# Optimization experiments

Measured on AMD Instinct MI355X. Metric: run time of the kernel, lower is better.

Reference implementation:

```python
import jax, jax.numpy as jnp
import numpy as np

N_HEAD = 16
D_MODEL = 1024
T_DIM = 64
# Faithful to torch source: temperature = d_model // n_head ** 0.5  ==  d_model // (n_head**0.5)
TEMPERATURE = D_MODEL // (N_HEAD ** 0.5)  # 1024 // 4.0 = 256.0
LN_EPS = 1e-5


def setup_inputs() -> dict:
    key = jax.random.key(0)
    ks = jax.random.split(key, 10)
    B, S = 4, 2048
    w = 0.02  # weight scale to keep activations/logits in a sane range
    return {
        "q": jax.random.normal(ks[0], (B, S, D_MODEL), jnp.float32),
        "k": jax.random.normal(ks[1], (B, S, D_MODEL), jnp.float32),
        "v": jax.random.normal(ks[2], (B, S, D_MODEL), jnp.float32),
        "t": jax.random.normal(ks[3], (B, T_DIM), jnp.float32),
        "w_q": jax.random.normal(ks[4], (D_MODEL, D_MODEL), jnp.float32) * w,
        "w_k": jax.random.normal(ks[5], (D_MODEL, D_MODEL), jnp.float32) * w,
        "w_v": jax.random.normal(ks[6], (D_MODEL, D_MODEL), jnp.float32) * w,
        "w_fc": jax.random.normal(ks[7], (D_MODEL, D_MODEL), jnp.float32) * w,
        "ada_w": jax.random.normal(ks[8], (2 * D_MODEL, T_DIM), jnp.float32) * w,
        "ada_b": jax.random.normal(ks[9], (2 * D_MODEL,), jnp.float32) * w,
    }


def _ada_layer_norm(x, t_emb, ada_w, ada_b):
    # linear(gelu(t_emb)) -> [B, 2*d]; exact (erf) GELU as in torch nn.GELU default
    emb = jax.nn.gelu(t_emb, approximate=False) @ ada_w.T + ada_b
    emb = emb[:, None, :]  # [B, 1, 2*d]
    scale, shift = jnp.split(emb, 2, axis=-1)
    mean = jnp.mean(x, axis=-1, keepdims=True)
    var = jnp.var(x, axis=-1, keepdims=True)
    ln = (x - mean) * jax.lax.rsqrt(var + LN_EPS)
    return ln * (1.0 + scale) + shift


def reference(q, k, v, t, w_q, w_k, w_v, w_fc, ada_w, ada_b):
    B, Sq, D = q.shape
    Sk = k.shape[1]
    H, Dk = N_HEAD, D // N_HEAD

    q = _ada_layer_norm(q, t, ada_w, ada_b)
    residual = q

    # projections (torch Linear, no bias): y = x @ W.T
    qh = (q @ w_q.T).reshape(B, Sq, H, Dk).transpose(0, 2, 1, 3)  # [B,H,Sq,Dk]
    kh = (k @ w_k.T).reshape(B, Sk, H, Dk).transpose(0, 2, 1, 3)
    vh = (v @ w_v.T).reshape(B, Sk, H, Dk).transpose(0, 2, 1, 3)

    scores = jnp.einsum("bhqd,bhkd->bhqk", qh, kh) / TEMPERATURE
    attn = jax.nn.softmax(scores, axis=-1)
    out = jnp.einsum("bhqk,bhkd->bhqd", attn, vh)  # [B,H,Sq,Dk]

    out = out.transpose(0, 2, 1, 3).reshape(B, Sq, D)
    out = out @ w_fc.T  # dropout is identity in eval
    return out + residual
```

## Files before the change

kernel.cpp:

```cpp
#include <hip/hip_runtime.h>
#include <hip/hip_bf16.h>
#include <cstdint>

typedef short bf16x8 __attribute__((ext_vector_type(8)));
typedef float f32x4  __attribute__((ext_vector_type(4)));
typedef unsigned short u16x8 __attribute__((ext_vector_type(8)));
typedef unsigned short u16x4 __attribute__((ext_vector_type(4)));

#define SEQ    2048
#define BATCH  4
#define DMODEL 1024
#define NHEAD  16
#define DKH    64
#define MROWS  (BATCH * SEQ)

__device__ __forceinline__ unsigned short f2bf(float f) {
  union { float f; uint32_t u; } x; x.f = f;
  uint32_t r = (x.u + 0x7fffu + ((x.u >> 16) & 1u)) >> 16;
  return (unsigned short)r;
}
__device__ __forceinline__ float bf2f(unsigned short u) {
  union { uint32_t u; float f; } x; x.u = ((uint32_t)u) << 16;
  return x.f;
}
__device__ __forceinline__ void gload_lds16(const void* g, void* l) {
  __builtin_amdgcn_global_load_lds(
      (const __attribute__((address_space(1))) void*)g,
      (__attribute__((address_space(3))) void*)l, 16, 0, 0);
}

__global__ __launch_bounds__(256) void cast_f32_bf16(
    const float* __restrict__ in, unsigned short* __restrict__ out, int n) {
  int i = (blockIdx.x * 256 + threadIdx.x) * 4;
  if (i + 3 < n) {
    float4 v = *(const float4*)(in + i);
    u16x4 o;
    o[0] = f2bf(v.x); o[1] = f2bf(v.y); o[2] = f2bf(v.z); o[3] = f2bf(v.w);
    *(u16x4*)(out + i) = o;
  }
}

__global__ __launch_bounds__(256) void ada_emb_kernel(
    const float* __restrict__ t, const float* __restrict__ ada_w,
    const float* __restrict__ ada_b, float* __restrict__ emb) {
  int b = blockIdx.y;
  int j = blockIdx.x * 256 + threadIdx.x;
  __shared__ float g[64];
  if (threadIdx.x < 64) {
    float x = t[b * 64 + threadIdx.x];
    g[threadIdx.x] = x * 0.5f * (1.0f + erff(x * 0.70710678118654752f));
  }
  __syncthreads();
  float acc = ada_b[j];
  const float* wr = ada_w + (size_t)j * 64;
  #pragma unroll
  for (int i = 0; i < 64; ++i) acc += g[i] * wr[i];
  emb[b * 2048 + j] = acc;
}

__global__ __launch_bounds__(256) void adaln_kernel(
    const float* __restrict__ q, const float* __restrict__ emb,
    unsigned short* __restrict__ xbf) {
  int row = blockIdx.x;
  int b = row >> 11;
  int tid = threadIdx.x;
  float4 x = ((const float4*)(q + (size_t)row * DMODEL))[tid];
  float s  = x.x + x.y + x.z + x.w;
  float s2 = x.x * x.x + x.y * x.y + x.z * x.z + x.w * x.w;
  #pragma unroll
  for (int off = 32; off > 0; off >>= 1) {
    s  += __shfl_down(s, off);
    s2 += __shfl_down(s2, off);
  }
  __shared__ float red[8];
  int w = tid >> 6;
  if ((tid & 63) == 0) { red[w * 2] = s; red[w * 2 + 1] = s2; }
  __syncthreads();
  s  = red[0] + red[2] + red[4] + red[6];
  s2 = red[1] + red[3] + red[5] + red[7];
  float mean = s * (1.0f / 1024.0f);
  float var  = s2 * (1.0f / 1024.0f) - mean * mean;
  float rs = rsqrtf(var + 1e-5f);
  float4 sc = ((const float4*)(emb + (size_t)b * 2048))[tid];
  float4 sh = ((const float4*)(emb + (size_t)b * 2048 + 1024))[tid];
  u16x4 o;
  o[0] = f2bf((x.x - mean) * rs * (1.0f + sc.x) + sh.x);
  o[1] = f2bf((x.y - mean) * rs * (1.0f + sc.y) + sh.y);
  o[2] = f2bf((x.z - mean) * rs * (1.0f + sc.z) + sh.z);
  o[3] = f2bf((x.w - mean) * rs * (1.0f + sc.w) + sh.w);
  ((u16x4*)(xbf + (size_t)row * DMODEL))[tid] = o;
}

template <int MODE>
__global__ __launch_bounds__(256) void gemm_bt(
    const unsigned short* __restrict__ A, const unsigned short* __restrict__ Bw,
    unsigned short* __restrict__ Cb, const unsigned short* __restrict__ resid,
    float* __restrict__ Cf) {
  __shared__ __align__(16) unsigned short Al[128 * 64];
  __shared__ __align__(16) unsigned short Bl[128 * 64];
  int tid = threadIdx.x;
  int lane = tid & 63, w = tid >> 6;
  int l15 = lane & 15, l16 = lane >> 4;
  int m0 = blockIdx.y * 128, n0 = blockIdx.x * 128;
  int wr = w >> 1, wc = w & 1;

  f32x4 acc[4][4];
  #pragma unroll
  for (int m = 0; m < 4; ++m)
    #pragma unroll
    for (int n = 0; n < 4; ++n) acc[m][n] = {0.f, 0.f, 0.f, 0.f};

  const unsigned short* Ab = A + (size_t)m0 * 1024;
  const unsigned short* Bb = Bw + (size_t)n0 * 1024;

  for (int kt = 0; kt < 16; ++kt) {
    int k0 = kt * 64;
    #pragma unroll
    for (int it = 0; it < 4; ++it) {
      int c = it * 256 + tid;
      int r = c >> 3, cg = c & 7;
      gload_lds16(Ab + (size_t)r * 1024 + k0 + cg * 8, &Al[c * 8]);
    }
    #pragma unroll
    for (int it = 0; it < 4; ++it) {
      int c = it * 256 + tid;
      int r = c >> 3, cg = c & 7;
      gload_lds16(Bb + (size_t)r * 1024 + k0 + cg * 8, &Bl[c * 8]);
    }
    __syncthreads();
    #pragma unroll
    for (int kk = 0; kk < 2; ++kk) {
      bf16x8 af[4], bfr[4];
      #pragma unroll
      for (int m = 0; m < 4; ++m)
        af[m] = *(const bf16x8*)&Al[(wr * 64 + m * 16 + l15) * 64 + kk * 32 + l16 * 8];
      #pragma unroll
      for (int n = 0; n < 4; ++n)
        bfr[n] = *(const bf16x8*)&Bl[(wc * 64 + n * 16 + l15) * 64 + kk * 32 + l16 * 8];
      #pragma unroll
      for (int m = 0; m < 4; ++m)
        #pragma unroll
        for (int n = 0; n < 4; ++n)
          acc[m][n] = __builtin_amdgcn_mfma_f32_16x16x32_bf16(af[m], bfr[n], acc[m][n], 0, 0, 0);
    }
    __syncthreads();
  }

  #pragma unroll
  for (int m = 0; m < 4; ++m) {
    #pragma unroll
    for (int r = 0; r < 4; ++r) {
      int row = m0 + wr * 64 + m * 16 + l16 * 4 + r;
      size_t base = (size_t)row * 1024 + n0 + wc * 64 + l15;
      #pragma unroll
      for (int n = 0; n < 4; ++n) {
        float val = acc[m][n][r];
        if (MODE == 0) {
          Cb[base + n * 16] = f2bf(val);
        } else {
          Cf[base + n * 16] = val + bf2f(resid[base + n * 16]);
        }
      }
    }
  }
}

__global__ __launch_bounds__(256) void attn_kernel(
    const unsigned short* __restrict__ Q, const unsigned short* __restrict__ K,
    const unsigned short* __restrict__ V, unsigned short* __restrict__ O) {
  int tid = threadIdx.x;
  int lane = tid & 63, w = tid >> 6;
  int l15 = lane & 15, l16 = lane >> 4;
  int sw7 = l15 & 7;

  int wgid = blockIdx.x;
  int e = (wgid & 7) * 128 + (wgid >> 3);
  int qt = e & 15, h = (e >> 4) & 15, b = e >> 8;

  __shared__ __align__(16) unsigned short Kl[64 * 64];
  __shared__ __align__(16) unsigned short VT[64 * 64];
  __shared__ __align__(16) unsigned short Pl[4][16 * 64];

  size_t hb = (size_t)b * SEQ * DMODEL + (size_t)h * DKH;
  int qrow = qt * 128 + w * 32;

  bf16x8 qf[2][2];
  #pragma unroll
  for (int qs = 0; qs < 2; ++qs)
    #pragma unroll
    for (int kk = 0; kk < 2; ++kk)
      qf[qs][kk] = *(const bf16x8*)(Q + hb + (size_t)(qrow + qs * 16 + l15) * DMODEL + kk * 32 + l16 * 8);

  float m_s[2] = {-INFINITY, -INFINITY};
  float l_s[2] = {0.f, 0.f};
  f32x4 oacc[2][4];
  #pragma unroll
  for (int qs = 0; qs < 2; ++qs)
    #pragma unroll
    for (int mm = 0; mm < 4; ++mm) oacc[qs][mm] = {0.f, 0.f, 0.f, 0.f};

  const float sc = 1.0f / 256.0f;

  for (int t = 0; t < SEQ / 64; ++t) {
    int kv0 = t * 64;
    #pragma unroll
    for (int it = 0; it < 2; ++it) {
      int c = it * 256 + tid;
      int r = c >> 3, cg = c & 7;
      gload_lds16(K + hb + (size_t)(kv0 + r) * DMODEL + (cg ^ (r & 7)) * 8, &Kl[c * 8]);
    }
    {
      int kv = lane, dk0 = w * 16;
      const unsigned short* vp = V + hb + (size_t)(kv0 + kv) * DMODEL + dk0;
      u16x8 v0 = *(const u16x8*)vp;
      u16x8 v1 = *(const u16x8*)(vp + 8);
      int kvhi = kv >> 3, kvlo = kv & 7;
      #pragma unroll
      for (int e2 = 0; e2 < 8; ++e2) {
        int d = dk0 + e2;
        VT[d * 64 + ((kvhi ^ (d & 7)) << 3) + kvlo] = v0[e2];
      }
      #pragma unroll
      for (int e2 = 0; e2 < 8; ++e2) {
        int d = dk0 + 8 + e2;
        VT[d * 64 + ((kvhi ^ (d & 7)) << 3) + kvlo] = v1[e2];
      }
    }
    __syncthreads();

    bf16x8 kf[2][4], vf[2][4];
    #pragma unroll
    for (int kk = 0; kk < 2; ++kk)
      #pragma unroll
      for (int n = 0; n < 4; ++n)
        kf[kk][n] = *(const bf16x8*)&Kl[(n * 16 + l15) * 64 + (((kk * 4 + l16) ^ sw7) << 3)];
    #pragma unroll
    for (int kk = 0; kk < 2; ++kk)
      #pragma unroll
      for (int mm = 0; mm < 4; ++mm)
        vf[kk][mm] = *(const bf16x8*)&VT[(mm * 16 + l15) * 64 + (((kk * 4 + l16) ^ sw7) << 3)];

    #pragma unroll
    for (int qs = 0; qs < 2; ++qs) {
      f32x4 sa[4];
      #pragma unroll
      for (int n = 0; n < 4; ++n) sa[n] = {0.f, 0.f, 0.f, 0.f};
      #pragma unroll
      for (int kk = 0; kk < 2; ++kk)
        #pragma unroll
        for (int n = 0; n < 4; ++n)
          sa[n] = __builtin_amdgcn_mfma_f32_16x16x32_bf16(kf[kk][n], qf[qs][kk], sa[n], 0, 0, 0);

      float pmax = -INFINITY;
      #pragma unroll
      for (int n = 0; n < 4; ++n)
        #pragma unroll
        for (int r = 0; r < 4; ++r) { sa[n][r] *= sc; pmax = fmaxf(pmax, sa[n][r]); }
      pmax = fmaxf(pmax, __shfl_xor(pmax, 16));
      pmax = fmaxf(pmax, __shfl_xor(pmax, 32));
      float mn = fmaxf(m_s[qs], pmax);
      float corr = __expf(m_s[qs] - mn);
      m_s[qs] = mn;
      float rsum = 0.f;
      #pragma unroll
      for (int n = 0; n < 4; ++n)
        #pragma unroll
        for (int r = 0; r < 4; ++r) { sa[n][r] = __expf(sa[n][r] - mn); rsum += sa[n][r]; }
      rsum += __shfl_xor(rsum, 16);
      rsum += __shfl_xor(rsum, 32);
      l_s[qs] = l_s[qs] * corr + rsum;
      #pragma unroll
      for (int mm = 0; mm < 4; ++mm)
        #pragma unroll
        for (int r = 0; r < 4; ++r) oacc[qs][mm][r] *= corr;

      #pragma unroll
      for (int n = 0; n < 4; ++n) {
        #pragma unroll
        for (int r0 = 0; r0 < 4; r0 += 2) {
          uint32_t pw = (uint32_t)f2bf(sa[n][r0]) | ((uint32_t)f2bf(sa[n][r0 + 1]) << 16);
          int idx = l15 * 64 + (((n * 2 + (l16 >> 1)) ^ sw7) << 3) + (l16 & 1) * 4 + r0;
          *(uint32_t*)&Pl[w][idx] = pw;
        }
      }
      bf16x8 pf[2];
      #pragma unroll
      for (int kk = 0; kk < 2; ++kk)
        pf[kk] = *(const bf16x8*)&Pl[w][l15 * 64 + (((kk * 4 + l16) ^ sw7) << 3)];

      #pragma unroll
      for (int kk = 0; kk < 2; ++kk)
        #pragma unroll
        for (int mm = 0; mm < 4; ++mm)
          oacc[qs][mm] = __builtin_amdgcn_mfma_f32_16x16x32_bf16(vf[kk][mm], pf[kk], oacc[qs][mm], 0, 0, 0);
    }
    __syncthreads();
  }

  #pragma unroll
  for (int qs = 0; qs < 2; ++qs) {
    float inv = 1.0f / l_s[qs];
    #pragma unroll
    for (int mm = 0; mm < 4; ++mm) {
      u16x4 ov;
      #pragma unroll
      for (int r = 0; r < 4; ++r) ov[r] = f2bf(oacc[qs][mm][r] * inv);
      *(u16x4*)(O + hb + (size_t)(qrow + qs * 16 + l15) * DMODEL + mm * 16 + l16 * 4) = ov;
    }
  }
}

static constexpr size_t EMB_OFF = 0;
static constexpr size_t WQ_OFF  = 32768;
static constexpr size_t WK_OFF  = WQ_OFF + 2097152;
static constexpr size_t WV_OFF  = WK_OFF + 2097152;
static constexpr size_t WFC_OFF = WV_OFF + 2097152;
static constexpr size_t XBF_OFF = WFC_OFF + 2097152;
static constexpr size_t KBF_OFF = XBF_OFF + 16777216;
static constexpr size_t VBF_OFF = KBF_OFF + 16777216;
static constexpr size_t QH_OFF  = VBF_OFF + 16777216;
static constexpr size_t KH_OFF  = QH_OFF + 16777216;
static constexpr size_t VH_OFF  = KH_OFF + 16777216;
static constexpr size_t ATTN_OFF = KBF_OFF;

extern "C" void kernel_launch(void* const* d_in, const int* in_sizes, int n_in,
                              void* d_out, int out_size, void* d_ws, size_t ws_size,
                              hipStream_t stream) {
  const float* q     = (const float*)d_in[0];
  const float* k     = (const float*)d_in[1];
  const float* v     = (const float*)d_in[2];
  const float* t     = (const float*)d_in[3];
  const float* w_q   = (const float*)d_in[4];
  const float* w_k   = (const float*)d_in[5];
  const float* w_v   = (const float*)d_in[6];
  const float* w_fc  = (const float*)d_in[7];
  const float* ada_w = (const float*)d_in[8];
  const float* ada_b = (const float*)d_in[9];

  char* ws = (char*)d_ws;
  float* emb           = (float*)(ws + EMB_OFF);
  unsigned short* wqb  = (unsigned short*)(ws + WQ_OFF);
  unsigned short* wkb  = (unsigned short*)(ws + WK_OFF);
  unsigned short* wvb  = (unsigned short*)(ws + WV_OFF);
  unsigned short* wfcb = (unsigned short*)(ws + WFC_OFF);
  unsigned short* xbf  = (unsigned short*)(ws + XBF_OFF);
  unsigned short* kbf  = (unsigned short*)(ws + KBF_OFF);
  unsigned short* vbf  = (unsigned short*)(ws + VBF_OFF);
  unsigned short* qh   = (unsigned short*)(ws + QH_OFF);
  unsigned short* kh   = (unsigned short*)(ws + KH_OFF);
  unsigned short* vh   = (unsigned short*)(ws + VH_OFF);
  unsigned short* attn = (unsigned short*)(ws + ATTN_OFF);
  float* outf          = (float*)d_out;

  cast_f32_bf16<<<1024, 256, 0, stream>>>(w_q,  wqb,  1048576);
  cast_f32_bf16<<<1024, 256, 0, stream>>>(w_k,  wkb,  1048576);
  cast_f32_bf16<<<1024, 256, 0, stream>>>(w_v,  wvb,  1048576);
  cast_f32_bf16<<<1024, 256, 0, stream>>>(w_fc, wfcb, 1048576);
  cast_f32_bf16<<<8192, 256, 0, stream>>>(k, kbf, 8388608);
  cast_f32_bf16<<<8192, 256, 0, stream>>>(v, vbf, 8388608);

  ada_emb_kernel<<<dim3(8, 4), 256, 0, stream>>>(t, ada_w, ada_b, emb);

  adaln_kernel<<<8192, 256, 0, stream>>>(q, emb, xbf);

  gemm_bt<0><<<dim3(8, 64), 256, 0, stream>>>(xbf, wqb, qh, nullptr, nullptr);
  gemm_bt<0><<<dim3(8, 64), 256, 0, stream>>>(kbf, wkb, kh, nullptr, nullptr);
  gemm_bt<0><<<dim3(8, 64), 256, 0, stream>>>(vbf, wvb, vh, nullptr, nullptr);

  attn_kernel<<<1024, 256, 0, stream>>>(qh, kh, vh, attn);

  gemm_bt<1><<<dim3(8, 64), 256, 0, stream>>>(attn, wfcb, nullptr, xbf, outf);
}
```

Before: 460.0 us.

## Batch cast and QKV GEMM launches, add lazy softmax rescale and MFMA priority

Merges the six cast launches into two grid-batched kernels and the three QKV projection GEMMs into one launch with a z-dimension. In attention, the score scale is folded into an exp2 FMA, and the running-max rescale of the output accumulator is skipped unless the max grows past a threshold. Packed bf16 conversion uses v_cvt_pk_bf16_f32, and s_setprio is raised around MFMA blocks. The changes cut launch overhead, idle tail time between kernels, and per-tile softmax ALU work. The lazy rescale allows exp values up to about 2^5, which adds some bf16 precision risk in P, and the hardware instruction rounds differently from the software conversion.

```diff
diff --git a/kernel.cpp b/kernel.cpp
--- a/kernel.cpp
+++ b/kernel.cpp
@@ -23,21 +23,43 @@
   union { uint32_t u; float f; } x; x.u = ((uint32_t)u) << 16;
   return x.f;
 }
+__device__ __forceinline__ uint32_t pack_bf2(float lo, float hi) {
+  uint32_t r;
+  asm("v_cvt_pk_bf16_f32 %0, %1, %2" : "=v"(r) : "v"(lo), "v"(hi));
+  return r;
+}
 __device__ __forceinline__ void gload_lds16(const void* g, void* l) {
   __builtin_amdgcn_global_load_lds(
       (const __attribute__((address_space(1))) void*)g,
       (__attribute__((address_space(3))) void*)l, 16, 0, 0);
 }
 
-__global__ __launch_bounds__(256) void cast_f32_bf16(
-    const float* __restrict__ in, unsigned short* __restrict__ out, int n) {
+__global__ __launch_bounds__(256) void cast4_kernel(
+    const float* __restrict__ s0, const float* __restrict__ s1,
+    const float* __restrict__ s2, const float* __restrict__ s3,
+    unsigned short* __restrict__ d0, unsigned short* __restrict__ d1,
+    unsigned short* __restrict__ d2, unsigned short* __restrict__ d3) {
+  int z = blockIdx.y;
+  const float* in = z == 0 ? s0 : z == 1 ? s1 : z == 2 ? s2 : s3;
+  unsigned short* out = z == 0 ? d0 : z == 1 ? d1 : z == 2 ? d2 : d3;
   int i = (blockIdx.x * 256 + threadIdx.x) * 4;
-  if (i + 3 < n) {
-    float4 v = *(const float4*)(in + i);
-    u16x4 o;
-    o[0] = f2bf(v.x); o[1] = f2bf(v.y); o[2] = f2bf(v.z); o[3] = f2bf(v.w);
-    *(u16x4*)(out + i) = o;
-  }
+  float4 v = *(const float4*)(in + i);
+  u16x4 o;
+  o[0] = f2bf(v.x); o[1] = f2bf(v.y); o[2] = f2bf(v.z); o[3] = f2bf(v.w);
+  *(u16x4*)(out + i) = o;
+}
+
+__global__ __launch_bounds__(256) void cast2_kernel(
+    const float* __restrict__ s0, const float* __restrict__ s1,
+    unsigned short* __restrict__ d0, unsigned short* __restrict__ d1) {
+  int z = blockIdx.y;
+  const float* in = z == 0 ? s0 : s1;
+  unsigned short* out = z == 0 ? d0 : d1;
+  int i = (blockIdx.x * 256 + threadIdx.x) * 4;
+  float4 v = *(const float4*)(in + i);
+  u16x4 o;
+  o[0] = f2bf(v.x); o[1] = f2bf(v.y); o[2] = f2bf(v.z); o[3] = f2bf(v.w);
+  *(u16x4*)(out + i) = o;
 }
 
 __global__ __launch_bounds__(256) void ada_emb_kernel(
@@ -92,10 +114,9 @@
 }
 
 template <int MODE>
-__global__ __launch_bounds__(256) void gemm_bt(
-    const unsigned short* __restrict__ A, const unsigned short* __restrict__ Bw,
-    unsigned short* __restrict__ Cb, const unsigned short* __restrict__ resid,
-    float* __restrict__ Cf) {
+__device__ __forceinline__ void gemm_body(
+    const unsigned short* A, const unsigned short* Bw,
+    unsigned short* Cb, const unsigned short* resid, float* Cf) {
   __shared__ __align__(16) unsigned short Al[128 * 64];
   __shared__ __align__(16) unsigned short Bl[128 * 64];
   int tid = threadIdx.x;
@@ -137,11 +158,13 @@
       #pragma unroll
       for (int n = 0; n < 4; ++n)
         bfr[n] = *(const bf16x8*)&Bl[(wc * 64 + n * 16 + l15) * 64 + kk * 32 + l16 * 8];
+      __builtin_amdgcn_s_setprio(1);
       #pragma unroll
       for (int m = 0; m < 4; ++m)
         #pragma unroll
         for (int n = 0; n < 4; ++n)
           acc[m][n] = __builtin_amdgcn_mfma_f32_16x16x32_bf16(af[m], bfr[n], acc[m][n], 0, 0, 0);
+      __builtin_amdgcn_s_setprio(0);
     }
     __syncthreads();
   }
@@ -165,6 +188,23 @@
   }
 }
 
+__global__ __launch_bounds__(256) void gemm_qkv_kernel(
+    const unsigned short* xbf, const unsigned short* kbf, const unsigned short* vbf,
+    const unsigned short* wq, const unsigned short* wk, const unsigned short* wv,
+    unsigned short* qh, unsigned short* kh, unsigned short* vh) {
+  int z = blockIdx.z;
+  const unsigned short* A = z == 0 ? xbf : z == 1 ? kbf : vbf;
+  const unsigned short* B = z == 0 ? wq  : z == 1 ? wk  : wv;
+  unsigned short* C       = z == 0 ? qh  : z == 1 ? kh  : vh;
+  gemm_body<0>(A, B, C, nullptr, nullptr);
+}
+
+__global__ __launch_bounds__(256) void gemm_fc_kernel(
+    const unsigned short* attn, const unsigned short* wfc,
+    const unsigned short* resid, float* outf) {
+  gemm_body<1>(attn, wfc, nullptr, resid, outf);
+}
+
 __global__ __launch_bounds__(256) void attn_kernel(
     const unsigned short* __restrict__ Q, const unsigned short* __restrict__ K,
     const unsigned short* __restrict__ V, unsigned short* __restrict__ O) {
@@ -191,15 +231,17 @@
     for (int kk = 0; kk < 2; ++kk)
       qf[qs][kk] = *(const bf16x8*)(Q + hb + (size_t)(qrow + qs * 16 + l15) * DMODEL + kk * 32 + l16 * 8);
 
-  float m_s[2] = {-INFINITY, -INFINITY};
-  float l_s[2] = {0.f, 0.f};
+  const float csc = 1.44269504f / 256.0f;
+  const float THR = 1280.0f;
+
+  float m_s[2]  = {-INFINITY, -INFINITY};
+  float mc_s[2] = {-INFINITY, -INFINITY};
+  float l_s[2]  = {0.f, 0.f};
   f32x4 oacc[2][4];
   #pragma unroll
   for (int qs = 0; qs < 2; ++qs)
     #pragma unroll
     for (int mm = 0; mm < 4; ++mm) oacc[qs][mm] = {0.f, 0.f, 0.f, 0.f};
-
-  const float sc = 1.0f / 256.0f;
 
   for (int t = 0; t < SEQ / 64; ++t) {
     int kv0 = t * 64;
@@ -245,40 +287,49 @@
       f32x4 sa[4];
       #pragma unroll
       for (int n = 0; n < 4; ++n) sa[n] = {0.f, 0.f, 0.f, 0.f};
+      __builtin_amdgcn_s_setprio(1);
       #pragma unroll
       for (int kk = 0; kk < 2; ++kk)
         #pragma unroll
         for (int n = 0; n < 4; ++n)
           sa[n] = __builtin_amdgcn_mfma_f32_16x16x32_bf16(kf[kk][n], qf[qs][kk], sa[n], 0, 0, 0);
-
-      float pmax = -INFINITY;
-      #pragma unroll
-      for (int n = 0; n < 4; ++n)
-        #pragma unroll
-        for (int r = 0; r < 4; ++r) { sa[n][r] *= sc; pmax = fmaxf(pmax, sa[n][r]); }
+      __builtin_amdgcn_s_setprio(0);
+
+      float pmax = fmaxf(fmaxf(fmaxf(sa[0][0], sa[0][1]), fmaxf(sa[0][2], sa[0][3])),
+                         fmaxf(fmaxf(sa[1][0], sa[1][1]), fmaxf(sa[1][2], sa[1][3])));
+      pmax = fmaxf(pmax, fmaxf(fmaxf(fmaxf(sa[2][0], sa[2][1]), fmaxf(sa[2][2], sa[2][3])),
+                               fmaxf(fmaxf(sa[3][0], sa[3][1]), fmaxf(sa[3][2], sa[3][3]))));
       pmax = fmaxf(pmax, __shfl_xor(pmax, 16));
       pmax = fmaxf(pmax, __shfl_xor(pmax, 32));
-      float mn = fmaxf(m_s[qs], pmax);
-      float corr = __expf(m_s[qs] - mn);
-      m_s[qs] = mn;
+      if (!__all(pmax - m_s[qs] <= THR)) {
+        float mn = fmaxf(m_s[qs], pmax);
+        float corr = __builtin_exp2f((m_s[qs] - mn) * csc);
+        m_s[qs] = mn;
+        mc_s[qs] = mn * csc;
+        l_s[qs] *= corr;
+        #pragma unroll
+        for (int mm = 0; mm < 4; ++mm)
+          #pragma unroll
+          for (int r = 0; r < 4; ++r) oacc[qs][mm][r] *= corr;
+      }
+      float mc = mc_s[qs];
       float rsum = 0.f;
       #pragma unroll
       for (int n = 0; n < 4; ++n)
         #pragma unroll
-        for (int r = 0; r < 4; ++r) { sa[n][r] = __expf(sa[n][r] - mn); rsum += sa[n][r]; }
+        for (int r = 0; r < 4; ++r) {
+          sa[n][r] = __builtin_exp2f(__builtin_fmaf(sa[n][r], csc, -mc));
+          rsum += sa[n][r];
+        }
       rsum += __shfl_xor(rsum, 16);
       rsum += __shfl_xor(rsum, 32);
-      l_s[qs] = l_s[qs] * corr + rsum;
-      #pragma unroll
-      for (int mm = 0; mm < 4; ++mm)
-        #pragma unroll
-        for (int r = 0; r < 4; ++r) oacc[qs][mm][r] *= corr;
+      l_s[qs] += rsum;
 
       #pragma unroll
       for (int n = 0; n < 4; ++n) {
         #pragma unroll
         for (int r0 = 0; r0 < 4; r0 += 2) {
-          uint32_t pw = (uint32_t)f2bf(sa[n][r0]) | ((uint32_t)f2bf(sa[n][r0 + 1]) << 16);
+          uint32_t pw = pack_bf2(sa[n][r0], sa[n][r0 + 1]);
           int idx = l15 * 64 + (((n * 2 + (l16 >> 1)) ^ sw7) << 3) + (l16 & 1) * 4 + r0;
           *(uint32_t*)&Pl[w][idx] = pw;
         }
@@ -288,11 +339,13 @@
       for (int kk = 0; kk < 2; ++kk)
         pf[kk] = *(const bf16x8*)&Pl[w][l15 * 64 + (((kk * 4 + l16) ^ sw7) << 3)];
 
+      __builtin_amdgcn_s_setprio(1);
       #pragma unroll
       for (int kk = 0; kk < 2; ++kk)
         #pragma unroll
         for (int mm = 0; mm < 4; ++mm)
           oacc[qs][mm] = __builtin_amdgcn_mfma_f32_16x16x32_bf16(vf[kk][mm], pf[kk], oacc[qs][mm], 0, 0, 0);
+      __builtin_amdgcn_s_setprio(0);
     }
     __syncthreads();
   }
@@ -302,10 +355,10 @@
     float inv = 1.0f / l_s[qs];
     #pragma unroll
     for (int mm = 0; mm < 4; ++mm) {
-      u16x4 ov;
-      #pragma unroll
-      for (int r = 0; r < 4; ++r) ov[r] = f2bf(oacc[qs][mm][r] * inv);
-      *(u16x4*)(O + hb + (size_t)(qrow + qs * 16 + l15) * DMODEL + mm * 16 + l16 * 4) = ov;
+      uint32_t w0 = pack_bf2(oacc[qs][mm][0] * inv, oacc[qs][mm][1] * inv);
+      uint32_t w1 = pack_bf2(oacc[qs][mm][2] * inv, oacc[qs][mm][3] * inv);
+      uint2 ov = {w0, w1};
+      *(uint2*)(O + hb + (size_t)(qrow + qs * 16 + l15) * DMODEL + mm * 16 + l16 * 4) = ov;
     }
   }
 }
@@ -352,22 +405,16 @@
   unsigned short* attn = (unsigned short*)(ws + ATTN_OFF);
   float* outf          = (float*)d_out;
 
-  cast_f32_bf16<<<1024, 256, 0, stream>>>(w_q,  wqb,  1048576);
-  cast_f32_bf16<<<1024, 256, 0, stream>>>(w_k,  wkb,  1048576);
-  cast_f32_bf16<<<1024, 256, 0, stream>>>(w_v,  wvb,  1048576);
-  cast_f32_bf16<<<1024, 256, 0, stream>>>(w_fc, wfcb, 1048576);
-  cast_f32_bf16<<<8192, 256, 0, stream>>>(k, kbf, 8388608);
-  cast_f32_bf16<<<8192, 256, 0, stream>>>(v, vbf, 8388608);
+  cast4_kernel<<<dim3(1024, 4), 256, 0, stream>>>(w_q, w_k, w_v, w_fc, wqb, wkb, wvb, wfcb);
+  cast2_kernel<<<dim3(8192, 2), 256, 0, stream>>>(k, v, kbf, vbf);
 
   ada_emb_kernel<<<dim3(8, 4), 256, 0, stream>>>(t, ada_w, ada_b, emb);
 
   adaln_kernel<<<8192, 256, 0, stream>>>(q, emb, xbf);
 
-  gemm_bt<0><<<dim3(8, 64), 256, 0, stream>>>(xbf, wqb, qh, nullptr, nullptr);
-  gemm_bt<0><<<dim3(8, 64), 256, 0, stream>>>(kbf, wkb, kh, nullptr, nullptr);
-  gemm_bt<0><<<dim3(8, 64), 256, 0, stream>>>(vbf, wvb, vh, nullptr, nullptr);
+  gemm_qkv_kernel<<<dim3(8, 64, 3), 256, 0, stream>>>(xbf, kbf, vbf, wqb, wkb, wvb, qh, kh, vh);
 
   attn_kernel<<<1024, 256, 0, stream>>>(qh, kh, vh, attn);
 
-  gemm_bt<1><<<dim3(8, 64), 256, 0, stream>>>(attn, wfcb, nullptr, xbf, outf);
-}
+  gemm_fc_kernel<<<dim3(8, 64), 256, 0, stream>>>(attn, wfcb, xbf, outf);
+}
```

After: 435.7 us. 1.06x faster.
